# Performance work log

Measured on AMD Instinct MI355X. Metric: run time of the kernel, lower is better.

Reference implementation:

```python
import jax, jax.numpy as jnp
import numpy as np

EPS = 1e-6
CLIP_RATIO = 1.0  # input_clip_ratio


def fwht(x):
    """Fast Walsh-Hadamard transform along last dim (N must be a power of 2).
    Unnormalized; caller divides by sqrt(N) (QuaRot OnlineHadamard convention)."""
    m, n = x.shape
    h = 1
    y = x
    while h < n:  # log2(n) fixed iterations, fine under jit
        y = y.reshape(m, n // (2 * h), 2, h)
        a, b = y[:, :, 0, :], y[:, :, 1, :]
        y = jnp.concatenate([a + b, a - b], axis=-1)  # [m, n//(2h), 2h]
        h *= 2
    return y.reshape(m, n)


def setup_inputs() -> dict:
    key = jax.random.key(0)
    k1, k2, k3 = jax.random.split(key, 3)
    M, IN, OUT = 8192, 4096, 4096
    x = jax.random.normal(k1, (M, IN), dtype=jnp.float32)
    weight = jax.random.normal(k2, (OUT, IN), dtype=jnp.float32) * 0.02
    bias = jax.random.normal(k3, (OUT,), dtype=jnp.float32) * 0.01
    return {"x": x, "weight": weight, "bias": bias}


def reference(x, weight, bias):
    # --- offline weight quantization (quantize_from_float) ---
    # per-output-row symmetric int4: scale = max|w| / 7, clamp min 1e-6
    w_scales = jnp.clip(jnp.max(jnp.abs(weight), axis=1, keepdims=True), EPS, None) / 7.0  # [OUT,1]
    qw = jnp.clip(jnp.round(weight / w_scales), -8, 7)  # int4 values kept in fp32 (exact)

    # --- online Hadamard rotation of activations ---
    n = x.shape[-1]
    x2 = fwht(x) * (1.0 / jnp.sqrt(jnp.float32(n)))

    # --- symmetric per-token int4 activation quantization (QuaRot Quantizer) ---
    sx = jnp.clip(jnp.max(jnp.abs(x2), axis=-1, keepdims=True), EPS, None) * (CLIP_RATIO / 7.0)  # [M,1]
    qx = jnp.clip(jnp.round(x2 / sx), -8, 7)

    qy = jnp.einsum('mk,nk->mn', qx, qw)  # [M, OUT]

    # --- sym_dequant: row scale (activation) * column scale (weight) + bias ---
    y = qy * sx * w_scales.T + bias[None, :]
    return y
```

## Files before the change

### kernel.cpp

```cpp
#include <hip/hip_runtime.h>
#include <hip/hip_bf16.h>
#include <cstdint>

#define QEPS 1e-6f

typedef int v4i __attribute__((ext_vector_type(4)));
typedef int v8i __attribute__((ext_vector_type(8)));
typedef float v4f __attribute__((ext_vector_type(4)));

__device__ __forceinline__ void gl_lds16(const void* g, void* l) {
  __builtin_amdgcn_global_load_lds(
      (const __attribute__((address_space(1))) void*)g,
      (__attribute__((address_space(3))) void*)l, 16, 0, 0);
}

__device__ __forceinline__ uint8_t enc_e4m3(float q) {
  const int idx = (int)q + 8;
  const unsigned long long lo = 0xB8C0C4C8CACCCED0ull;
  const unsigned long long hi = 0x4E4C4A4844403800ull;
  const unsigned long long tbl = (idx < 8) ? lo : hi;
  return (uint8_t)(tbl >> ((idx & 7) * 8));
}

__global__ __launch_bounds__(256) void wquant_kernel(const float* __restrict__ w,
                                                     uint8_t* __restrict__ qw,
                                                     float* __restrict__ wscale) {
  const int n = blockIdx.x;
  const int t = threadIdx.x;
  const float4* wrow = (const float4*)(w + (size_t)n * 4096);
  float4 v[4];
  float am = 0.f;
#pragma unroll
  for (int i = 0; i < 4; ++i) {
    v[i] = wrow[i * 256 + t];
    am = fmaxf(am, fmaxf(fmaxf(fabsf(v[i].x), fabsf(v[i].y)),
                         fmaxf(fabsf(v[i].z), fabsf(v[i].w))));
  }
#pragma unroll
  for (int off = 32; off > 0; off >>= 1)
    am = fmaxf(am, __shfl_down(am, off));
  __shared__ float wm[4];
  if ((t & 63) == 0) wm[t >> 6] = am;
  __syncthreads();
  const float rowmax = fmaxf(fmaxf(wm[0], wm[1]), fmaxf(wm[2], wm[3]));
  const float scale = fmaxf(rowmax, QEPS) / 7.0f;
  if (t == 0) wscale[n] = scale;
  uchar4* qrow = (uchar4*)(qw + (size_t)n * 4096);
#pragma unroll
  for (int i = 0; i < 4; ++i) {
    uchar4 q;
    q.x = enc_e4m3(fminf(fmaxf(rintf(v[i].x / scale), -8.f), 7.f));
    q.y = enc_e4m3(fminf(fmaxf(rintf(v[i].y / scale), -8.f), 7.f));
    q.z = enc_e4m3(fminf(fmaxf(rintf(v[i].z / scale), -8.f), 7.f));
    q.w = enc_e4m3(fminf(fmaxf(rintf(v[i].w / scale), -8.f), 7.f));
    qrow[i * 256 + t] = q;
  }
}

__global__ __launch_bounds__(256) void xquant_kernel(const float* __restrict__ x,
                                                     uint8_t* __restrict__ qx,
                                                     float* __restrict__ sx) {
  const int m = blockIdx.x * 4 + (threadIdx.x >> 6);
  const int g = threadIdx.x & 63;
  const float4* xrow = (const float4*)(x + (size_t)m * 4096);
  float4 v[16];
#pragma unroll
  for (int j = 0; j < 16; ++j) v[j] = xrow[j * 64 + g];

#pragma unroll
  for (int j = 0; j < 16; ++j) {
    float a0 = v[j].x, b0 = v[j].y, a1 = v[j].z, b1 = v[j].w;
    v[j].x = a0 + b0; v[j].y = a0 - b0;
    v[j].z = a1 + b1; v[j].w = a1 - b1;
  }
#pragma unroll
  for (int j = 0; j < 16; ++j) {
    float a0 = v[j].x, b0 = v[j].z, a1 = v[j].y, b1 = v[j].w;
    v[j].x = a0 + b0; v[j].z = a0 - b0;
    v[j].y = a1 + b1; v[j].w = a1 - b1;
  }
#pragma unroll
  for (int d = 1; d < 64; d <<= 1) {
    const bool low = (g & d) == 0;
#pragma unroll
    for (int j = 0; j < 16; ++j) {
      float px = __shfl_xor(v[j].x, d);
      float py = __shfl_xor(v[j].y, d);
      float pz = __shfl_xor(v[j].z, d);
      float pw = __shfl_xor(v[j].w, d);
      v[j].x = low ? (v[j].x + px) : (px - v[j].x);
      v[j].y = low ? (v[j].y + py) : (py - v[j].y);
      v[j].z = low ? (v[j].z + pz) : (pz - v[j].z);
      v[j].w = low ? (v[j].w + pw) : (pw - v[j].w);
    }
  }
#pragma unroll
  for (int d = 1; d < 16; d <<= 1) {
#pragma unroll
    for (int j = 0; j < 16; ++j) {
      if ((j & d) == 0) {
        float4 a = v[j], b = v[j + d];
        v[j].x = a.x + b.x; v[j].y = a.y + b.y;
        v[j].z = a.z + b.z; v[j].w = a.w + b.w;
        v[j + d].x = a.x - b.x; v[j + d].y = a.y - b.y;
        v[j + d].z = a.z - b.z; v[j + d].w = a.w - b.w;
      }
    }
  }

  float am = 0.f;
#pragma unroll
  for (int j = 0; j < 16; ++j)
    am = fmaxf(am, fmaxf(fmaxf(fabsf(v[j].x), fabsf(v[j].y)),
                         fmaxf(fabsf(v[j].z), fabsf(v[j].w))));
#pragma unroll
  for (int off = 32; off > 0; off >>= 1)
    am = fmaxf(am, __shfl_xor(am, off));

  const float inv64 = 1.0f / 64.0f;
  const float sxv = fmaxf(am * inv64, QEPS) * (1.0f / 7.0f);
  if (g == 0) sx[m] = sxv;

  uchar4* qrow = (uchar4*)(qx + (size_t)m * 4096);
#pragma unroll
  for (int j = 0; j < 16; ++j) {
    uchar4 q;
    q.x = enc_e4m3(fminf(fmaxf(rintf((v[j].x * inv64) / sxv), -8.f), 7.f));
    q.y = enc_e4m3(fminf(fmaxf(rintf((v[j].y * inv64) / sxv), -8.f), 7.f));
    q.z = enc_e4m3(fminf(fmaxf(rintf((v[j].z * inv64) / sxv), -8.f), 7.f));
    q.w = enc_e4m3(fminf(fmaxf(rintf((v[j].w * inv64) / sxv), -8.f), 7.f));
    qrow[j * 64 + g] = q;
  }
}

#define BM 128
#define BN 128
#define BK 128

__global__ __launch_bounds__(256) void gemm_kernel(const uint8_t* __restrict__ qx,
                                                   const uint8_t* __restrict__ qw,
                                                   const float* __restrict__ sx,
                                                   const float* __restrict__ wscale,
                                                   const float* __restrict__ bias,
                                                   float* __restrict__ out) {
  __shared__ uint8_t As[BM * BK] __attribute__((aligned(16)));
  __shared__ uint8_t Bs[BN * BK] __attribute__((aligned(16)));
  const int t = threadIdx.x;
  const int m0 = blockIdx.y * BM;
  const int n0 = blockIdx.x * BN;
  const int lane = t & 63;
  const int wave = t >> 6;
  const int wr = wave >> 1;
  const int wc = wave & 1;
  const int lr = lane & 15;
  const int lq = lane >> 4;

  v4f acc[4][4] = {};

  const int rA = t >> 3;
  const int csrc16 = (((t & 7) ^ (rA & 7)) << 4);
  const uint8_t* ga = qx + (size_t)(m0 + rA) * 4096 + csrc16;
  const uint8_t* gb = qw + (size_t)(n0 + rA) * 4096 + csrc16;
  const int ldst = t * 16;

  const int r7 = lr & 7;
  int aoff0[4], aoff1[4], boff0[4], boff1[4];
#pragma unroll
  for (int i = 0; i < 4; ++i) {
    const int rowa = (wr * 64 + i * 16 + lr) * 128;
    const int rowb = (wc * 64 + i * 16 + lr) * 128;
    aoff0[i] = rowa + (((2 * lq) ^ r7) << 4);
    aoff1[i] = rowa + (((2 * lq + 1) ^ r7) << 4);
    boff0[i] = rowb + (((2 * lq) ^ r7) << 4);
    boff1[i] = rowb + (((2 * lq + 1) ^ r7) << 4);
  }

  for (int k0 = 0; k0 < 4096; k0 += BK) {
    __syncthreads();
#pragma unroll
    for (int i = 0; i < 4; ++i) {
      gl_lds16(ga + k0 + (size_t)i * 32 * 4096, As + i * 4096 + ldst);
      gl_lds16(gb + k0 + (size_t)i * 32 * 4096, Bs + i * 4096 + ldst);
    }
    __syncthreads();

    union frag { v8i v; v4i h[2]; };
    frag a[4], b[4];
#pragma unroll
    for (int i = 0; i < 4; ++i) {
      a[i].h[0] = *(const v4i*)(As + aoff0[i]);
      a[i].h[1] = *(const v4i*)(As + aoff1[i]);
      b[i].h[0] = *(const v4i*)(Bs + boff0[i]);
      b[i].h[1] = *(const v4i*)(Bs + boff1[i]);
    }
#pragma unroll
    for (int mt = 0; mt < 4; ++mt)
#pragma unroll
      for (int nt = 0; nt < 4; ++nt)
        acc[mt][nt] = __builtin_amdgcn_mfma_scale_f32_16x16x128_f8f6f4(
            a[mt].v, b[nt].v, acc[mt][nt],
            0, 0,
            0, 0x7F7F7F7F,
            0, 0x7F7F7F7F);
  }

#pragma unroll
  for (int mt = 0; mt < 4; ++mt) {
#pragma unroll
    for (int r = 0; r < 4; ++r) {
      const int m = m0 + wr * 64 + mt * 16 + lq * 4 + r;
      const float sm = sx[m];
#pragma unroll
      for (int nt = 0; nt < 4; ++nt) {
        const int n = n0 + wc * 64 + nt * 16 + lr;
        out[(size_t)m * 4096 + n] = acc[mt][nt][r] * sm * wscale[n] + bias[n];
      }
    }
  }
}

extern "C" void kernel_launch(void* const* d_in, const int* in_sizes, int n_in,
                              void* d_out, int out_size, void* d_ws, size_t ws_size,
                              hipStream_t stream) {
  const float* x = (const float*)d_in[0];
  const float* w = (const float*)d_in[1];
  const float* bias = (const float*)d_in[2];
  float* out = (float*)d_out;

  uint8_t* qx = (uint8_t*)d_ws;
  uint8_t* qw = qx + (size_t)8192 * 4096;
  float* wscale = (float*)(qw + (size_t)4096 * 4096);
  float* sxp = wscale + 4096;

  wquant_kernel<<<4096, 256, 0, stream>>>(w, qw, wscale);
  xquant_kernel<<<2048, 256, 0, stream>>>(x, qx, sxp);
  dim3 grid(4096 / BN, 8192 / BM);
  gemm_kernel<<<grid, 256, 0, stream>>>(qx, qw, sxp, wscale, bias, out);
}
```

Before: 418.2 us.

## Enlarge GEMM tile to 256x256 with double-buffered LDS and block swizzle

The GEMM moves to 256x256 tiles with 8 waves. Shared memory is double-buffered so the global-to-LDS load for the next K step is issued while MFMAs run on the current buffer. MFMA work is split into quadrants with barriers and raised s_setprio, and a block-index swizzle is added to improve L2 reuse. This targets the load stalls and low data reuse of the single-buffered 128x128 kernel, at the cost of more registers and LDS (128KB) per block, which may limit occupancy.

```diff
diff --git a/kernel.cpp b/kernel.cpp
--- a/kernel.cpp
+++ b/kernel.cpp
@@ -1,5 +1,4 @@
 #include <hip/hip_runtime.h>
-#include <hip/hip_bf16.h>
 #include <cstdint>
 
 #define QEPS 1e-6f
@@ -133,87 +132,149 @@
   }
 }
 
-#define BM 128
-#define BN 128
+#define BM 256
+#define BN 256
 #define BK 128
 
-__global__ __launch_bounds__(256) void gemm_kernel(const uint8_t* __restrict__ qx,
-                                                   const uint8_t* __restrict__ qw,
-                                                   const float* __restrict__ sx,
-                                                   const float* __restrict__ wscale,
-                                                   const float* __restrict__ bias,
-                                                   float* __restrict__ out) {
-  __shared__ uint8_t As[BM * BK] __attribute__((aligned(16)));
-  __shared__ uint8_t Bs[BN * BK] __attribute__((aligned(16)));
+union frag_u { v8i v; v4i h[2]; };
+
+#define MFMA_Q(MB, NB)                                                        \
+  do {                                                                        \
+    __builtin_amdgcn_s_setprio(1);                                            \
+    _Pragma("unroll") for (int i_ = 0; i_ < 4; ++i_)                          \
+        _Pragma("unroll") for (int j_ = 0; j_ < 2; ++j_)                      \
+            acc[(MB) + i_][(NB) + j_] =                                       \
+                __builtin_amdgcn_mfma_scale_f32_16x16x128_f8f6f4(             \
+                    a[i_].v, b[j_].v, acc[(MB) + i_][(NB) + j_], 0, 0, 0,     \
+                    0x7F7F7F7F, 0, 0x7F7F7F7F);                               \
+    __builtin_amdgcn_s_setprio(0);                                            \
+  } while (0)
+
+#define LDA4(BASE)                                                            \
+  do {                                                                        \
+    _Pragma("unroll") for (int i_ = 0; i_ < 4; ++i_) {                        \
+      const int o_ = arow[(BASE) + i_];                                       \
+      a[i_].h[0] = *(const v4i*)(As_c + o_);                                  \
+      a[i_].h[1] = *(const v4i*)(As_c + (o_ ^ 16));                           \
+    }                                                                         \
+  } while (0)
+
+#define LDB2(BASE)                                                            \
+  do {                                                                        \
+    _Pragma("unroll") for (int j_ = 0; j_ < 2; ++j_) {                        \
+      const int o_ = brow[(BASE) + j_];                                       \
+      b[j_].h[0] = *(const v4i*)(Bs_c + o_);                                  \
+      b[j_].h[1] = *(const v4i*)(Bs_c + (o_ ^ 16));                           \
+    }                                                                         \
+  } while (0)
+
+__global__ __launch_bounds__(512, 2) void gemm_kernel(const uint8_t* __restrict__ qx,
+                                                      const uint8_t* __restrict__ qw,
+                                                      const float* __restrict__ sx,
+                                                      const float* __restrict__ wscale,
+                                                      const float* __restrict__ bias,
+                                                      float* __restrict__ out) {
+  __shared__ uint8_t As[2][BM * BK] __attribute__((aligned(16)));
+  __shared__ uint8_t Bs[2][BN * BK] __attribute__((aligned(16)));
+
   const int t = threadIdx.x;
-  const int m0 = blockIdx.y * BM;
-  const int n0 = blockIdx.x * BN;
+  const int bid = blockIdx.y * gridDim.x + blockIdx.x;
+  const int swz = ((bid & 7) << 6) | (bid >> 3);
+  const int bx = swz & 15;
+  const int by = swz >> 4;
+  const int m0 = by * BM;
+  const int n0 = bx * BN;
+
   const int lane = t & 63;
   const int wave = t >> 6;
-  const int wr = wave >> 1;
-  const int wc = wave & 1;
+  const int wr = wave >> 2;
+  const int wc = wave & 3;
   const int lr = lane & 15;
   const int lq = lane >> 4;
-
-  v4f acc[4][4] = {};
+  const int r7 = lr & 7;
+  const int c0 = ((2 * lq) ^ r7) << 4;
+
+  v4f acc[8][4] = {};
 
   const int rA = t >> 3;
-  const int csrc16 = (((t & 7) ^ (rA & 7)) << 4);
-  const uint8_t* ga = qx + (size_t)(m0 + rA) * 4096 + csrc16;
-  const uint8_t* gb = qw + (size_t)(n0 + rA) * 4096 + csrc16;
+  const int csrc = (((t & 7) ^ (rA & 7)) << 4);
+  const uint8_t* ga = qx + (size_t)(m0 + rA) * 4096 + csrc;
+  const uint8_t* gb = qw + (size_t)(n0 + rA) * 4096 + csrc;
   const int ldst = t * 16;
 
-  const int r7 = lr & 7;
-  int aoff0[4], aoff1[4], boff0[4], boff1[4];
-#pragma unroll
-  for (int i = 0; i < 4; ++i) {
-    const int rowa = (wr * 64 + i * 16 + lr) * 128;
-    const int rowb = (wc * 64 + i * 16 + lr) * 128;
-    aoff0[i] = rowa + (((2 * lq) ^ r7) << 4);
-    aoff1[i] = rowa + (((2 * lq + 1) ^ r7) << 4);
-    boff0[i] = rowb + (((2 * lq) ^ r7) << 4);
-    boff1[i] = rowb + (((2 * lq + 1) ^ r7) << 4);
-  }
-
-  for (int k0 = 0; k0 < 4096; k0 += BK) {
+  int arow[8], brow[4];
+#pragma unroll
+  for (int mt = 0; mt < 8; ++mt)
+    arow[mt] = (wr * 128 + mt * 16 + lr) * BK + c0;
+#pragma unroll
+  for (int nt = 0; nt < 4; ++nt)
+    brow[nt] = (wc * 64 + nt * 16 + lr) * BK + c0;
+
+#pragma unroll
+  for (int s = 0; s < 4; ++s) {
+    gl_lds16(ga + (size_t)s * 64 * 4096, As[0] + s * 8192 + ldst);
+    gl_lds16(gb + (size_t)s * 64 * 4096, Bs[0] + s * 8192 + ldst);
+  }
+  __syncthreads();
+
+  for (int kt = 0; kt < 32; ++kt) {
+    const uint8_t* As_c = As[kt & 1];
+    const uint8_t* Bs_c = Bs[kt & 1];
+    frag_u a[4], b[2];
+
+    LDA4(0);
+    LDB2(0);
+    if (kt < 31) {
+      const int koff = (kt + 1) << 7;
+      uint8_t* Ad = As[(kt & 1) ^ 1];
+      uint8_t* Bd = Bs[(kt & 1) ^ 1];
+#pragma unroll
+      for (int s = 0; s < 4; ++s) {
+        gl_lds16(ga + (size_t)s * 64 * 4096 + koff, Ad + s * 8192 + ldst);
+        gl_lds16(gb + (size_t)s * 64 * 4096 + koff, Bd + s * 8192 + ldst);
+      }
+    }
+    __builtin_amdgcn_s_barrier();
+    asm volatile("s_waitcnt lgkmcnt(0)" ::: "memory");
+    MFMA_Q(0, 0);
+    __builtin_amdgcn_s_barrier();
+
+    LDB2(2);
+    __builtin_amdgcn_s_barrier();
+    asm volatile("s_waitcnt lgkmcnt(0)" ::: "memory");
+    MFMA_Q(0, 2);
+    __builtin_amdgcn_s_barrier();
+
+    LDA4(4);
+    __builtin_amdgcn_s_barrier();
+    asm volatile("s_waitcnt lgkmcnt(0)" ::: "memory");
+    MFMA_Q(4, 2);
+    __builtin_amdgcn_s_barrier();
+
+    LDB2(0);
+    __builtin_amdgcn_s_barrier();
+    asm volatile("s_waitcnt lgkmcnt(0)" ::: "memory");
+    MFMA_Q(4, 0);
     __syncthreads();
-#pragma unroll
-    for (int i = 0; i < 4; ++i) {
-      gl_lds16(ga + k0 + (size_t)i * 32 * 4096, As + i * 4096 + ldst);
-      gl_lds16(gb + k0 + (size_t)i * 32 * 4096, Bs + i * 4096 + ldst);
-    }
-    __syncthreads();
-
-    union frag { v8i v; v4i h[2]; };
-    frag a[4], b[4];
-#pragma unroll
-    for (int i = 0; i < 4; ++i) {
-      a[i].h[0] = *(const v4i*)(As + aoff0[i]);
-      a[i].h[1] = *(const v4i*)(As + aoff1[i]);
-      b[i].h[0] = *(const v4i*)(Bs + boff0[i]);
-      b[i].h[1] = *(const v4i*)(Bs + boff1[i]);
-    }
-#pragma unroll
-    for (int mt = 0; mt < 4; ++mt)
-#pragma unroll
-      for (int nt = 0; nt < 4; ++nt)
-        acc[mt][nt] = __builtin_amdgcn_mfma_scale_f32_16x16x128_f8f6f4(
-            a[mt].v, b[nt].v, acc[mt][nt],
-            0, 0,
-            0, 0x7F7F7F7F,
-            0, 0x7F7F7F7F);
-  }
-
-#pragma unroll
-  for (int mt = 0; mt < 4; ++mt) {
+  }
+
+  float wv[4], bv[4];
+#pragma unroll
+  for (int nt = 0; nt < 4; ++nt) {
+    const int n = n0 + wc * 64 + nt * 16 + lr;
+    wv[nt] = wscale[n];
+    bv[nt] = bias[n];
+  }
+#pragma unroll
+  for (int mt = 0; mt < 8; ++mt) {
 #pragma unroll
     for (int r = 0; r < 4; ++r) {
-      const int m = m0 + wr * 64 + mt * 16 + lq * 4 + r;
+      const int m = m0 + wr * 128 + mt * 16 + lq * 4 + r;
       const float sm = sx[m];
 #pragma unroll
       for (int nt = 0; nt < 4; ++nt) {
         const int n = n0 + wc * 64 + nt * 16 + lr;
-        out[(size_t)m * 4096 + n] = acc[mt][nt][r] * sm * wscale[n] + bias[n];
+        out[(size_t)m * 4096 + n] = acc[mt][nt][r] * sm * wv[nt] + bv[nt];
       }
     }
   }
@@ -235,5 +296,5 @@
   wquant_kernel<<<4096, 256, 0, stream>>>(w, qw, wscale);
   xquant_kernel<<<2048, 256, 0, stream>>>(x, qx, sxp);
   dim3 grid(4096 / BN, 8192 / BM);
-  gemm_kernel<<<grid, 256, 0, stream>>>(qx, qw, sxp, wscale, bias, out);
-}
+  gemm_kernel<<<grid, 512, 0, stream>>>(qx, qw, sxp, wscale, bias, out);
+}
```

Result: no change. 424.1 us (+1.4%).
